# Kernel optimization log

Measured on AMD Instinct MI355X. Metric: run time of the kernel, lower is better.

Reference implementation:

```python
import jax, jax.numpy as jnp
import numpy as np

B, T, E, H = 16, 4096, 384, 64

def setup_inputs() -> dict:
    key = jax.random.key(0)
    k1, k2, k3, k4 = jax.random.split(key, 4)
    x = jax.random.normal(k1, (B, T, E), dtype=jnp.float32)
    # nn.Linear default init ~ U(-1/sqrt(fan_in), 1/sqrt(fan_in)); scale normals similarly
    s = 1.0 / np.sqrt(E)
    Wk = jax.random.uniform(k2, (E, H), dtype=jnp.float32, minval=-s, maxval=s)
    Wq = jax.random.uniform(k3, (E, H), dtype=jnp.float32, minval=-s, maxval=s)
    Wv = jax.random.uniform(k4, (E, H), dtype=jnp.float32, minval=-s, maxval=s)
    return {"x": x, "Wk": Wk, "Wq": Wq, "Wv": Wv}

def reference(x, Wk, Wq, Wv):
    b, t, c = x.shape
    k = x @ Wk          # [b,t,h]
    q = x @ Wq          # [b,t,h]
    v = x @ Wv          # [b,t,h]
    # scale by C**-0.5 where C is the embedding dim (as in source)
    scale = c ** (-0.5)
    weights = jnp.einsum('bqh,bkh->bqk', q, k) * scale  # [b,t,t]
    causal = jnp.tril(jnp.ones((t, t), dtype=bool))
    weights = jnp.where(causal, weights, -jnp.inf)
    weights = jax.nn.softmax(weights, axis=-1)
    # dropout is identity in eval mode
    out = jnp.einsum('bqk,bkh->bqh', weights, v)          # [b,t,h]
    return out
```

## Files before the change

### kernel.cpp

```cpp
#include <hip/hip_runtime.h>
#include <hip/hip_bf16.h>
#include <math.h>


typedef __attribute__((ext_vector_type(4))) float f32x4;
typedef __attribute__((ext_vector_type(8))) __bf16 bf16x8;

#define DEVI static __device__ __forceinline__

DEVI unsigned short f2bf(float f) {
  union { float f; unsigned int u; } x; x.f = f;
  unsigned int r = x.u + 0x7fffu + ((x.u >> 16) & 1u);
  return (unsigned short)(r >> 16);
}

DEVI unsigned int cvtpk_bf16(float lo, float hi) {
  unsigned int r;
  asm("v_cvt_pk_bf16_f32 %0, %1, %2" : "=v"(r) : "v"(lo), "v"(hi));
  return r;
}

DEVI f32x4 mfma16(bf16x8 a, bf16x8 b, f32x4 c) {
  return __builtin_amdgcn_mfma_f32_16x16x32_bf16(a, b, c, 0, 0, 0);
}

DEVI bf16x8 lds_frag(const unsigned short* buf, int row, int gran) {
  return *(const bf16x8*)(buf + row * 64 + ((gran ^ (row & 7)) << 3));
}

DEVI void gl_lds16(const unsigned short* g, unsigned short* l) {
  __builtin_amdgcn_global_load_lds(
      (const __attribute__((address_space(1))) unsigned int*)g,
      (__attribute__((address_space(3))) unsigned int*)l, 16, 0, 0);
}

__global__ __launch_bounds__(256) void k_pack(const float* __restrict__ Wk,
                                              const float* __restrict__ Wq,
                                              const float* __restrict__ Wv,
                                              unsigned short* __restrict__ WT) {
  int idx = blockIdx.x * 256 + threadIdx.x;
  if (idx >= 192 * 384) return;
  int n = idx / 384, k = idx - n * 384;
  const float* W = (n < 64) ? Wk : ((n < 128) ? Wq : Wv);
  float val = W[k * 64 + (n & 63)];
  if (n >= 64 && n < 128) val *= 0.073622223f;
  WT[idx] = f2bf(val);
}

__global__ __launch_bounds__(256, 4) void k_proj(const float* __restrict__ x,
                                                 const unsigned short* __restrict__ WT,
                                                 unsigned short* __restrict__ Y,
                                                 unsigned short* __restrict__ VT) {
  __shared__ __align__(16) unsigned short As[64 * 64];
  __shared__ __align__(16) unsigned short Bs[192 * 64];
  const int tid = threadIdx.x;
  const int lane = tid & 63, wid = tid >> 6;
  const int q = lane & 15, g = lane >> 4;
  const int wm = wid >> 1, wn = wid & 1;
  const int m0 = blockIdx.x * 64;

  f32x4 acc[2][6];
#pragma unroll
  for (int mt = 0; mt < 2; ++mt)
#pragma unroll
    for (int nt = 0; nt < 6; ++nt) acc[mt][nt] = f32x4{0.f, 0.f, 0.f, 0.f};

  const int ar = tid >> 2, ap = tid & 3;

  for (int ks = 0; ks < 6; ++ks) {
    const float4* xp = (const float4*)(x + (size_t)(m0 + ar) * 384 + ks * 64 + ap * 16);
#pragma unroll
    for (int cc = 0; cc < 2; ++cc) {
      float4 f0 = xp[cc * 2], f1 = xp[cc * 2 + 1];
      union { unsigned short h[8]; uint4 v; } u;
      u.h[0] = f2bf(f0.x); u.h[1] = f2bf(f0.y); u.h[2] = f2bf(f0.z); u.h[3] = f2bf(f0.w);
      u.h[4] = f2bf(f1.x); u.h[5] = f2bf(f1.y); u.h[6] = f2bf(f1.z); u.h[7] = f2bf(f1.w);
      int gran = ap * 2 + cc;
      *(uint4*)(As + ar * 64 + ((gran ^ (ar & 7)) << 3)) = u.v;
    }
#pragma unroll
    for (int i = 0; i < 6; ++i) {
      int c = tid + 256 * i;
      int row = c >> 3, gr = c & 7;
      uint4 w = *(const uint4*)(WT + (size_t)row * 384 + ks * 64 + gr * 8);
      *(uint4*)(Bs + row * 64 + ((gr ^ (row & 7)) << 3)) = w;
    }
    __syncthreads();
#pragma unroll
    for (int kk = 0; kk < 2; ++kk) {
      bf16x8 af[2], bfv[6];
#pragma unroll
      for (int mt = 0; mt < 2; ++mt) af[mt] = lds_frag(As, wm * 32 + mt * 16 + q, kk * 4 + g);
#pragma unroll
      for (int nt = 0; nt < 6; ++nt) bfv[nt] = lds_frag(Bs, wn * 96 + nt * 16 + q, kk * 4 + g);
#pragma unroll
      for (int mt = 0; mt < 2; ++mt)
#pragma unroll
        for (int nt = 0; nt < 6; ++nt) acc[mt][nt] = mfma16(af[mt], bfv[nt], acc[mt][nt]);
    }
    __syncthreads();
  }
#pragma unroll
  for (int mt = 0; mt < 2; ++mt) {
    const int mrow = m0 + wm * 32 + mt * 16 + g * 4;
#pragma unroll
    for (int nt = 0; nt < 6; ++nt) {
      const int ncol = wn * 96 + nt * 16 + q;
      if (wn == 1 && nt >= 2) {
        const int d = (nt - 2) * 16 + q;
        const int bb = mrow >> 12, t = mrow & 4095;
        uint2 pv;
        pv.x = cvtpk_bf16(acc[mt][nt][0], acc[mt][nt][1]);
        pv.y = cvtpk_bf16(acc[mt][nt][2], acc[mt][nt][3]);
        *(uint2*)(VT + (size_t)(bb * 64 + d) * 4096 + t) = pv;
      } else {
        size_t base = (size_t)mrow * 128 + ncol;
#pragma unroll
        for (int j = 0; j < 4; ++j) Y[base + (size_t)j * 128] = f2bf(acc[mt][nt][j]);
      }
    }
  }
}

__global__ __launch_bounds__(512, 4) void k_attn(const unsigned short* __restrict__ Y,
                                                 const unsigned short* __restrict__ VT,
                                                 float* __restrict__ out) {
  __shared__ __align__(16) unsigned short Ks[4][64 * 64];
  __shared__ __align__(16) unsigned short Vs[4][64 * 64];
  __shared__ __align__(16) unsigned short Ps[8][16 * 64];

  const int id = blockIdx.x;
  const int xcd = id & 7;
  const int b = xcd * 2 + ((id >> 3) & 1);
  const int rank = id >> 4;
  const int i = (rank < 16) ? (31 - rank) : (rank - 16);
  const int q0 = i * 128;
  const int nkv = 2 * i + 2;

  const int tid = threadIdx.x;
  const int lane = tid & 63, wid = tid >> 6;
  const int p = wid >> 2;
  const int w4 = wid & 3;
  const int q = lane & 15, g = lane >> 4;

  const unsigned short* Yb = Y + (size_t)b * 4096 * 128;
  const unsigned short* Vb = VT + (size_t)b * 64 * 4096;

#define STAGE(S, KV0)                                                           \
  {                                                                             \
    int r = tid >> 3, grs = (tid & 7) ^ (r & 7);                                \
    gl_lds16(Yb + (size_t)((KV0) + r) * 128 + grs * 8, Ks[S] + tid * 8);        \
    gl_lds16(Vb + (size_t)r * 4096 + (KV0) + grs * 8, Vs[S] + tid * 8);         \
  }

  STAGE(0, 0)
  STAGE(1, 64)
  __syncthreads();

  bf16x8 qf[2][2];
#pragma unroll
  for (int qh = 0; qh < 2; ++qh) {
    const unsigned short* qp = Yb + (size_t)(q0 + w4 * 32 + qh * 16 + q) * 128 + 64;
    qf[qh][0] = *(const bf16x8*)(qp + g * 8);
    qf[qh][1] = *(const bf16x8*)(qp + 32 + g * 8);
  }

  f32x4 accO[2][4];
#pragma unroll
  for (int qh = 0; qh < 2; ++qh)
#pragma unroll
    for (int dt = 0; dt < 4; ++dt) accO[qh][dt] = f32x4{0.f, 0.f, 0.f, 0.f};
  float lsum[2] = {0.f, 0.f};

  const int mytiles = 2 * i + 1 + (w4 >> 1);
  const int nIt = nkv >> 1;

  for (int it = 0; it < nIt; ++it) {
    const int kt = 2 * it + p;
    const int t2 = 2 * it + 2, t3 = 2 * it + 3;
    if (t2 < nkv) STAGE(t2 & 3, t2 * 64)
    if (t3 < nkv) STAGE(t3 & 3, t3 * 64)

    if (kt < mytiles) {
      const int kv0 = kt * 64;
      const unsigned short* Kc = Ks[kt & 3];
      const unsigned short* Vc = Vs[kt & 3];

      bf16x8 ka0[4], ka1[4];
#pragma unroll
      for (int t = 0; t < 4; ++t) {
        ka0[t] = lds_frag(Kc, t * 16 + q, g);
        ka1[t] = lds_frag(Kc, t * 16 + q, 4 + g);
      }
      f32x4 accS[2][4];
      __builtin_amdgcn_s_setprio(1);
#pragma unroll
      for (int qh = 0; qh < 2; ++qh)
#pragma unroll
        for (int t = 0; t < 4; ++t) {
          f32x4 z = f32x4{0.f, 0.f, 0.f, 0.f};
          z = mfma16(ka0[t], qf[qh][0], z);
          z = mfma16(ka1[t], qf[qh][1], z);
          accS[qh][t] = z;
        }
      __builtin_amdgcn_s_setprio(0);

      const bool dmw = (kv0 + 63 >= q0 + w4 * 32);
      bf16x8 bp[2][2];
#pragma unroll
      for (int qh = 0; qh < 2; ++qh) {
        if (dmw) {
          const int qrow = q0 + w4 * 32 + qh * 16 + q;
#pragma unroll
          for (int t = 0; t < 4; ++t)
#pragma unroll
            for (int j = 0; j < 4; ++j)
              if (kv0 + t * 16 + g * 4 + j > qrow) accS[qh][t][j] = -INFINITY;
        }
        float ps0 = 0.f, ps1 = 0.f;
#pragma unroll
        for (int t = 0; t < 4; ++t) {
          float p0 = __builtin_amdgcn_exp2f(accS[qh][t][0]);
          float p1 = __builtin_amdgcn_exp2f(accS[qh][t][1]);
          float p2 = __builtin_amdgcn_exp2f(accS[qh][t][2]);
          float p3 = __builtin_amdgcn_exp2f(accS[qh][t][3]);
          ps0 += p0 + p1;
          ps1 += p2 + p3;
          uint2 pv;
          pv.x = cvtpk_bf16(p0, p1);
          pv.y = cvtpk_bf16(p2, p3);
          *(uint2*)(Ps[wid] + q * 64 + ((t * 16 + g * 4) ^ ((q & 7) << 3))) = pv;
        }
        lsum[qh] += ps0 + ps1;
        asm volatile("" ::: "memory");
        bp[qh][0] = lds_frag(Ps[wid], q, g);
        bp[qh][1] = lds_frag(Ps[wid], q, 4 + g);
        asm volatile("" ::: "memory");
      }

      __builtin_amdgcn_s_setprio(1);
#pragma unroll
      for (int dt = 0; dt < 4; ++dt) {
        bf16x8 av0 = lds_frag(Vc, dt * 16 + q, g);
        bf16x8 av1 = lds_frag(Vc, dt * 16 + q, 4 + g);
#pragma unroll
        for (int qh = 0; qh < 2; ++qh) {
          accO[qh][dt] = mfma16(av0, bp[qh][0], accO[qh][dt]);
          accO[qh][dt] = mfma16(av1, bp[qh][1], accO[qh][dt]);
        }
      }
      __builtin_amdgcn_s_setprio(0);
    }

    __syncthreads();
  }
#undef STAGE

#pragma unroll
  for (int qh = 0; qh < 2; ++qh) {
    lsum[qh] += __shfl_xor(lsum[qh], 16);
    lsum[qh] += __shfl_xor(lsum[qh], 32);
  }

  float* scrO = (float*)Ks;
  float* scrL = (float*)Vs;
  const int si = (w4 * 64 + lane) * 2;
  if (p == 1) {
#pragma unroll
    for (int qh = 0; qh < 2; ++qh) {
      float* so = scrO + (si + qh) * 16;
#pragma unroll
      for (int dt = 0; dt < 4; ++dt) *(float4*)(so + dt * 4) = *(float4*)&accO[qh][dt];
      scrL[si + qh] = lsum[qh];
    }
  }
  __syncthreads();
  if (p == 0) {
#pragma unroll
    for (int qh = 0; qh < 2; ++qh) {
      const float* so = scrO + (si + qh) * 16;
      float rl = 1.0f / (lsum[qh] + scrL[si + qh]);
      const int qrow = q0 + w4 * 32 + qh * 16 + q;
      float* op = out + (size_t)(b * 4096 + qrow) * 64;
#pragma unroll
      for (int dt = 0; dt < 4; ++dt) {
        float4 ob = *(const float4*)(so + dt * 4);
        f32x4 vO;
        vO[0] = (accO[qh][dt][0] + ob.x) * rl;
        vO[1] = (accO[qh][dt][1] + ob.y) * rl;
        vO[2] = (accO[qh][dt][2] + ob.z) * rl;
        vO[3] = (accO[qh][dt][3] + ob.w) * rl;
        *(float4*)(op + dt * 16 + g * 4) = *(float4*)&vO;
      }
    }
  }
}

extern "C" void kernel_launch(void* const* d_in, const int* in_sizes, int n_in,
                              void* d_out, int out_size, void* d_ws, size_t ws_size,
                              hipStream_t stream) {
  const float* x  = (const float*)d_in[0];
  const float* Wk = (const float*)d_in[1];
  const float* Wq = (const float*)d_in[2];
  const float* Wv = (const float*)d_in[3];
  float* out = (float*)d_out;

  unsigned short* WT = (unsigned short*)d_ws;
  unsigned short* Y  = WT + 73728;
  unsigned short* VT = Y + 8388608;

  hipLaunchKernelGGL(k_pack, dim3(288), dim3(256), 0, stream, Wk, Wq, Wv, WT);
  hipLaunchKernelGGL(k_proj, dim3(1024), dim3(256), 0, stream, x, WT, Y, VT);
  hipLaunchKernelGGL(k_attn, dim3(512), dim3(512), 0, stream, Y, VT, out);
}
```

Before: 91.17 us.

## Permute K rows at staging to keep P in registers, dropping LDS round-trip

Rows of the K tile are loaded into LDS in a permuted order, so the S=K·Q MFMA output lands in registers already laid out as the B-operand fragment for the P·V MFMA. The per-wave Ps shared buffer, its writes, the barriers around it and the fragment reloads are all removed. The causal mask index arithmetic is updated to match the permuted key positions. This cuts LDS traffic and shared memory use, which could also raise occupancy, at the cost of a permutation that must exactly match the MFMA fragment layout.

```diff
diff --git a/kernel.cpp b/kernel.cpp
--- a/kernel.cpp
+++ b/kernel.cpp
@@ -127,7 +127,6 @@
                                                  float* __restrict__ out) {
   __shared__ __align__(16) unsigned short Ks[4][64 * 64];
   __shared__ __align__(16) unsigned short Vs[4][64 * 64];
-  __shared__ __align__(16) unsigned short Ps[8][16 * 64];
 
   const int id = blockIdx.x;
   const int xcd = id & 7;
@@ -149,7 +148,8 @@
 #define STAGE(S, KV0)                                                           \
   {                                                                             \
     int r = tid >> 3, grs = (tid & 7) ^ (r & 7);                                \
-    gl_lds16(Yb + (size_t)((KV0) + r) * 128 + grs * 8, Ks[S] + tid * 8);        \
+    int kp = (r & 32) | ((r & 12) << 1) | ((r & 16) >> 2) | (r & 3);            \
+    gl_lds16(Yb + (size_t)((KV0) + kp) * 128 + grs * 8, Ks[S] + tid * 8);       \
     gl_lds16(Vb + (size_t)r * 4096 + (KV0) + grs * 8, Vs[S] + tid * 8);         \
   }
 
@@ -214,28 +214,34 @@
 #pragma unroll
           for (int t = 0; t < 4; ++t)
 #pragma unroll
-            for (int j = 0; j < 4; ++j)
-              if (kv0 + t * 16 + g * 4 + j > qrow) accS[qh][t][j] = -INFINITY;
+            for (int j = 0; j < 4; ++j) {
+              const int kvl = ((t >> 1) << 5) + (g << 3) + ((t & 1) << 2) + j;
+              if (kv0 + kvl > qrow) accS[qh][t][j] = -INFINITY;
+            }
         }
+        float pp[4][4];
         float ps0 = 0.f, ps1 = 0.f;
 #pragma unroll
         for (int t = 0; t < 4; ++t) {
-          float p0 = __builtin_amdgcn_exp2f(accS[qh][t][0]);
-          float p1 = __builtin_amdgcn_exp2f(accS[qh][t][1]);
-          float p2 = __builtin_amdgcn_exp2f(accS[qh][t][2]);
-          float p3 = __builtin_amdgcn_exp2f(accS[qh][t][3]);
-          ps0 += p0 + p1;
-          ps1 += p2 + p3;
-          uint2 pv;
-          pv.x = cvtpk_bf16(p0, p1);
-          pv.y = cvtpk_bf16(p2, p3);
-          *(uint2*)(Ps[wid] + q * 64 + ((t * 16 + g * 4) ^ ((q & 7) << 3))) = pv;
+          pp[t][0] = __builtin_amdgcn_exp2f(accS[qh][t][0]);
+          pp[t][1] = __builtin_amdgcn_exp2f(accS[qh][t][1]);
+          pp[t][2] = __builtin_amdgcn_exp2f(accS[qh][t][2]);
+          pp[t][3] = __builtin_amdgcn_exp2f(accS[qh][t][3]);
+          ps0 += pp[t][0] + pp[t][1];
+          ps1 += pp[t][2] + pp[t][3];
         }
         lsum[qh] += ps0 + ps1;
-        asm volatile("" ::: "memory");
-        bp[qh][0] = lds_frag(Ps[wid], q, g);
-        bp[qh][1] = lds_frag(Ps[wid], q, 4 + g);
-        asm volatile("" ::: "memory");
+        uint4 u0, u1;
+        u0.x = cvtpk_bf16(pp[0][0], pp[0][1]);
+        u0.y = cvtpk_bf16(pp[0][2], pp[0][3]);
+        u0.z = cvtpk_bf16(pp[1][0], pp[1][1]);
+        u0.w = cvtpk_bf16(pp[1][2], pp[1][3]);
+        u1.x = cvtpk_bf16(pp[2][0], pp[2][1]);
+        u1.y = cvtpk_bf16(pp[2][2], pp[2][3]);
+        u1.z = cvtpk_bf16(pp[3][0], pp[3][1]);
+        u1.w = cvtpk_bf16(pp[3][2], pp[3][3]);
+        bp[qh][0] = __builtin_bit_cast(bf16x8, u0);
+        bp[qh][1] = __builtin_bit_cast(bf16x8, u1);
       }
 
       __builtin_amdgcn_s_setprio(1);
```

After: 86.57 us. -5.0%, faster.

## Permute K rows at staging to keep P in registers and interleave softmax with MFMA

Applied to the files above, without the earlier changes.

The K tile is now staged into LDS with a permuted row order, so the MFMA output layout of S lines up with the B-operand layout needed for the PV product. P can then be packed to bf16 directly in registers, which removes the per-wave Ps LDS round trip and its shared memory allocation. The two 16-row query halves are also software-pipelined: the QK MFMAs for the second half and the PV MFMAs for the first half are interleaved with the softmax of the other half. The cost is higher register pressure from holding V fragments and two S accumulators at once, and the causal mask indexing now depends on the permutation being correct.

```diff
diff --git a/kernel.cpp b/kernel.cpp
--- a/kernel.cpp
+++ b/kernel.cpp
@@ -127,7 +127,6 @@
                                                  float* __restrict__ out) {
   __shared__ __align__(16) unsigned short Ks[4][64 * 64];
   __shared__ __align__(16) unsigned short Vs[4][64 * 64];
-  __shared__ __align__(16) unsigned short Ps[8][16 * 64];
 
   const int id = blockIdx.x;
   const int xcd = id & 7;
@@ -149,7 +148,8 @@
 #define STAGE(S, KV0)                                                           \
   {                                                                             \
     int r = tid >> 3, grs = (tid & 7) ^ (r & 7);                                \
-    gl_lds16(Yb + (size_t)((KV0) + r) * 128 + grs * 8, Ks[S] + tid * 8);        \
+    int kp = (r & 32) | ((r & 12) << 1) | ((r & 16) >> 2) | (r & 3);            \
+    gl_lds16(Yb + (size_t)((KV0) + kp) * 128 + grs * 8, Ks[S] + tid * 8);       \
     gl_lds16(Vb + (size_t)r * 4096 + (KV0) + grs * 8, Vs[S] + tid * 8);         \
   }
 
@@ -174,6 +174,40 @@
 
   const int mytiles = 2 * i + 1 + (w4 >> 1);
   const int nIt = nkv >> 1;
+
+#define SOFTMAX(QH, ACC, BP0, BP1)                                              \
+  {                                                                             \
+    if (dmw) {                                                                  \
+      const int qrow = q0 + w4 * 32 + (QH) * 16 + q;                            \
+      _Pragma("unroll") for (int t = 0; t < 4; ++t)                             \
+        _Pragma("unroll") for (int j = 0; j < 4; ++j) {                         \
+          const int kvl = ((t >> 1) << 5) + (g << 3) + ((t & 1) << 2) + j;      \
+          if (kv0 + kvl > qrow) (ACC)[t][j] = -INFINITY;                        \
+        }                                                                       \
+    }                                                                           \
+    float pp[4][4];                                                             \
+    float ps0 = 0.f, ps1 = 0.f;                                                 \
+    _Pragma("unroll") for (int t = 0; t < 4; ++t) {                             \
+      pp[t][0] = __builtin_amdgcn_exp2f((ACC)[t][0]);                           \
+      pp[t][1] = __builtin_amdgcn_exp2f((ACC)[t][1]);                           \
+      pp[t][2] = __builtin_amdgcn_exp2f((ACC)[t][2]);                           \
+      pp[t][3] = __builtin_amdgcn_exp2f((ACC)[t][3]);                           \
+      ps0 += pp[t][0] + pp[t][1];                                               \
+      ps1 += pp[t][2] + pp[t][3];                                               \
+    }                                                                           \
+    lsum[QH] += ps0 + ps1;                                                      \
+    uint4 u0, u1;                                                               \
+    u0.x = cvtpk_bf16(pp[0][0], pp[0][1]);                                      \
+    u0.y = cvtpk_bf16(pp[0][2], pp[0][3]);                                      \
+    u0.z = cvtpk_bf16(pp[1][0], pp[1][1]);                                      \
+    u0.w = cvtpk_bf16(pp[1][2], pp[1][3]);                                      \
+    u1.x = cvtpk_bf16(pp[2][0], pp[2][1]);                                      \
+    u1.y = cvtpk_bf16(pp[2][2], pp[2][3]);                                      \
+    u1.z = cvtpk_bf16(pp[3][0], pp[3][1]);                                      \
+    u1.w = cvtpk_bf16(pp[3][2], pp[3][3]);                                      \
+    (BP0) = __builtin_bit_cast(bf16x8, u0);                                     \
+    (BP1) = __builtin_bit_cast(bf16x8, u1);                                     \
+  }
 
   for (int it = 0; it < nIt; ++it) {
     const int kt = 2 * it + p;
@@ -185,6 +219,7 @@
       const int kv0 = kt * 64;
       const unsigned short* Kc = Ks[kt & 3];
       const unsigned short* Vc = Vs[kt & 3];
+      const bool dmw = (kv0 + 63 >= q0 + w4 * 32);
 
       bf16x8 ka0[4], ka1[4];
 #pragma unroll
@@ -192,69 +227,60 @@
         ka0[t] = lds_frag(Kc, t * 16 + q, g);
         ka1[t] = lds_frag(Kc, t * 16 + q, 4 + g);
       }
-      f32x4 accS[2][4];
+      bf16x8 av0[4], av1[4];
+#pragma unroll
+      for (int dt = 0; dt < 4; ++dt) {
+        av0[dt] = lds_frag(Vc, dt * 16 + q, g);
+        av1[dt] = lds_frag(Vc, dt * 16 + q, 4 + g);
+      }
+
+      f32x4 accS0[4];
       __builtin_amdgcn_s_setprio(1);
 #pragma unroll
-      for (int qh = 0; qh < 2; ++qh)
-#pragma unroll
-        for (int t = 0; t < 4; ++t) {
-          f32x4 z = f32x4{0.f, 0.f, 0.f, 0.f};
-          z = mfma16(ka0[t], qf[qh][0], z);
-          z = mfma16(ka1[t], qf[qh][1], z);
-          accS[qh][t] = z;
-        }
+      for (int t = 0; t < 4; ++t) {
+        f32x4 z = f32x4{0.f, 0.f, 0.f, 0.f};
+        z = mfma16(ka0[t], qf[0][0], z);
+        z = mfma16(ka1[t], qf[0][1], z);
+        accS0[t] = z;
+      }
       __builtin_amdgcn_s_setprio(0);
 
-      const bool dmw = (kv0 + 63 >= q0 + w4 * 32);
-      bf16x8 bp[2][2];
-#pragma unroll
-      for (int qh = 0; qh < 2; ++qh) {
-        if (dmw) {
-          const int qrow = q0 + w4 * 32 + qh * 16 + q;
-#pragma unroll
-          for (int t = 0; t < 4; ++t)
-#pragma unroll
-            for (int j = 0; j < 4; ++j)
-              if (kv0 + t * 16 + g * 4 + j > qrow) accS[qh][t][j] = -INFINITY;
-        }
-        float ps0 = 0.f, ps1 = 0.f;
-#pragma unroll
-        for (int t = 0; t < 4; ++t) {
-          float p0 = __builtin_amdgcn_exp2f(accS[qh][t][0]);
-          float p1 = __builtin_amdgcn_exp2f(accS[qh][t][1]);
-          float p2 = __builtin_amdgcn_exp2f(accS[qh][t][2]);
-          float p3 = __builtin_amdgcn_exp2f(accS[qh][t][3]);
-          ps0 += p0 + p1;
-          ps1 += p2 + p3;
-          uint2 pv;
-          pv.x = cvtpk_bf16(p0, p1);
-          pv.y = cvtpk_bf16(p2, p3);
-          *(uint2*)(Ps[wid] + q * 64 + ((t * 16 + g * 4) ^ ((q & 7) << 3))) = pv;
-        }
-        lsum[qh] += ps0 + ps1;
-        asm volatile("" ::: "memory");
-        bp[qh][0] = lds_frag(Ps[wid], q, g);
-        bp[qh][1] = lds_frag(Ps[wid], q, 4 + g);
-        asm volatile("" ::: "memory");
-      }
-
+      bf16x8 bp00, bp01;
+      SOFTMAX(0, accS0, bp00, bp01)
+
+      f32x4 accS1[4];
       __builtin_amdgcn_s_setprio(1);
 #pragma unroll
+      for (int t = 0; t < 4; ++t) {
+        f32x4 z = f32x4{0.f, 0.f, 0.f, 0.f};
+        z = mfma16(ka0[t], qf[1][0], z);
+        z = mfma16(ka1[t], qf[1][1], z);
+        accS1[t] = z;
+      }
+
+#pragma unroll
       for (int dt = 0; dt < 4; ++dt) {
-        bf16x8 av0 = lds_frag(Vc, dt * 16 + q, g);
-        bf16x8 av1 = lds_frag(Vc, dt * 16 + q, 4 + g);
-#pragma unroll
-        for (int qh = 0; qh < 2; ++qh) {
-          accO[qh][dt] = mfma16(av0, bp[qh][0], accO[qh][dt]);
-          accO[qh][dt] = mfma16(av1, bp[qh][1], accO[qh][dt]);
-        }
+        accO[0][dt] = mfma16(av0[dt], bp00, accO[0][dt]);
+        accO[0][dt] = mfma16(av1[dt], bp01, accO[0][dt]);
       }
       __builtin_amdgcn_s_setprio(0);
+
+      bf16x8 bp10, bp11;
+      SOFTMAX(1, accS1, bp10, bp11)
+
+      __builtin_amdgcn_s_setprio(1);
+#pragma unroll
+      for (int dt = 0; dt < 4; ++dt) {
+        accO[1][dt] = mfma16(av0[dt], bp10, accO[1][dt]);
+        accO[1][dt] = mfma16(av1[dt], bp11, accO[1][dt]);
+      }
+      __builtin_amdgcn_s_setprio(0);
     }
 
     __syncthreads();
   }
 #undef STAGE
+#undef SOFTMAX
 
 #pragma unroll
   for (int qh = 0; qh < 2; ++qh) {
```

Measured after the change: 186.0 us. +104.0%, slower.
